# Kernel optimization log

Measured on AMD Instinct MI355X. Metric: run time of the kernel, lower is better.

The kernel has to match this reference:

```python
import jax, jax.numpy as jnp
import numpy as np

B = 512        # number of graphs in the batch
NP = 512       # nodes per graph (max segment length)
N = B * NP     # total nodes
D = 256        # in_feats
K = 32         # top-k nodes kept per graph


def setup_inputs() -> dict:
    key = jax.random.key(0)
    k1, k2 = jax.random.split(key, 2)
    feat = jax.random.normal(k1, (N, D), dtype=jnp.float32)
    w = jax.random.normal(k2, (1, D), dtype=jnp.float32) / np.sqrt(D)  # nn.Linear(in_feats, 1) weight
    b = jnp.zeros((1,), dtype=jnp.float32)                              # nn.Linear bias
    segment_ids = jnp.repeat(jnp.arange(B, dtype=jnp.int32), NP)        # sorted graph id per node
    return {"feat": feat, "w": w, "b": b, "segment_ids": segment_ids}


def reference(feat, w, b, segment_ids):
    # gate = self.att(feat) -> (N, 1) -> (N,)
    gate = (feat @ w.T + b)[:, 0]

    # dgl.softmax_nodes: numerically stable segment softmax per graph
    gmax = jax.ops.segment_max(gate, segment_ids, num_segments=B)
    e = jnp.exp(gate - gmax[segment_ids])
    denom = jax.ops.segment_sum(e, segment_ids, num_segments=B)
    gate_sm = e / denom[segment_ids]                                    # (N,)

    # position of each node within its segment (supports ragged segments)
    counts = jax.ops.segment_sum(jnp.ones((N,), jnp.int32), segment_ids, num_segments=B)
    offsets = jnp.concatenate([jnp.zeros((1,), jnp.int32), jnp.cumsum(counts)[:-1].astype(jnp.int32)])
    pos = jnp.arange(N, dtype=jnp.int32) - offsets[segment_ids]

    # scatter gates into dense (B, NP) padded with -inf, keep node ids alongside
    neg_inf = jnp.finfo(jnp.float32).min
    dense_gate = jnp.full((B, NP), neg_inf, jnp.float32).at[segment_ids, pos].set(gate_sm)
    dense_nid = jnp.zeros((B, NP), jnp.int32).at[segment_ids, pos].set(jnp.arange(N, dtype=jnp.int32))

    # dgl.topk_nodes: per-graph top-k by gate, gather node features -> (B, K, D)
    _, cols = jax.lax.top_k(dense_gate, K)
    node_idx = jnp.take_along_axis(dense_nid, cols, axis=1)             # (B, K) global node ids
    return feat[node_idx]                                               # (B, K, D)
```

## Files before the change

### kernel.cpp

```cpp
#include <hip/hip_runtime.h>

#define D   256
#define NP  512
#define BG  512
#define K   32
#define D4  (D/4)

__global__ __launch_bounds__(256) void gate_kernel(const float* __restrict__ feat,
                                                   const float* __restrict__ w,
                                                   const float* __restrict__ b,
                                                   float* __restrict__ gate,
                                                   int n_rows) {
    const int lane   = threadIdx.x & 63;
    const int wave   = (blockIdx.x * blockDim.x + threadIdx.x) >> 6;
    const int nwaves = (gridDim.x * blockDim.x) >> 6;

    const float4 w4  = ((const float4*)w)[lane];
    const float bias = b[0];
    const float4* f4 = (const float4*)feat;

    for (int row = wave; row < n_rows; row += nwaves) {
        float4 f = f4[(size_t)row * D4 + lane];
        float s = f.x * w4.x + f.y * w4.y + f.z * w4.z + f.w * w4.w;
        #pragma unroll
        for (int off = 32; off; off >>= 1)
            s += __shfl_xor(s, off, 64);
        if (lane == 0) gate[row] = s + bias;
    }
}

__global__ __launch_bounds__(256) void topk_kernel(const float* __restrict__ feat,
                                                   const float* __restrict__ gate,
                                                   float* __restrict__ out) {
    __shared__ float sval[NP];
    __shared__ int   sidx[NP];
    __shared__ float red[4];
    __shared__ float s_bcast;

    const int g    = blockIdx.x;
    const int tid  = threadIdx.x;
    const int lane = tid & 63;
    const int wid  = tid >> 6;

    const float v0 = gate[g * NP + tid];
    const float v1 = gate[g * NP + tid + 256];

    float m = fmaxf(v0, v1);
    #pragma unroll
    for (int off = 32; off; off >>= 1)
        m = fmaxf(m, __shfl_xor(m, off, 64));
    if (lane == 0) red[wid] = m;
    __syncthreads();
    if (tid == 0) s_bcast = fmaxf(fmaxf(red[0], red[1]), fmaxf(red[2], red[3]));
    __syncthreads();
    const float gmax = s_bcast;

    const float e0 = expf(v0 - gmax);
    const float e1 = expf(v1 - gmax);
    float s = e0 + e1;
    #pragma unroll
    for (int off = 32; off; off >>= 1)
        s += __shfl_xor(s, off, 64);
    __syncthreads();
    if (lane == 0) red[wid] = s;
    __syncthreads();
    if (tid == 0) s_bcast = (red[0] + red[1]) + (red[2] + red[3]);
    __syncthreads();
    const float denom = s_bcast;

    sval[tid]        = e0 / denom;  sidx[tid]        = tid;
    sval[tid + 256]  = e1 / denom;  sidx[tid + 256]  = tid + 256;
    __syncthreads();

    for (int k = 2; k <= NP; k <<= 1) {
        for (int j = k >> 1; j > 0; j >>= 1) {
            #pragma unroll
            for (int rep = 0; rep < 2; ++rep) {
                int t = tid + rep * 256;
                int ixj = t ^ j;
                if (ixj > t) {
                    float va = sval[t],  vb = sval[ixj];
                    int   ia = sidx[t],  ib = sidx[ixj];
                    bool b_first = (vb > va) || (vb == va && ib < ia);
                    bool do_swap = ((t & k) == 0) ? b_first : !b_first;
                    if (do_swap) {
                        sval[t] = vb; sval[ixj] = va;
                        sidx[t] = ib; sidx[ixj] = ia;
                    }
                }
            }
            __syncthreads();
        }
    }

    const float4* f4 = (const float4*)feat;
    float4*       o4 = (float4*)out;
    #pragma unroll
    for (int q = tid; q < K * D4; q += 256) {
        int r = q >> 6;
        int c = q & 63;
        int node = g * NP + sidx[r];
        o4[((size_t)(g * K + r)) * D4 + c] = f4[(size_t)node * D4 + c];
    }
}

extern "C" void kernel_launch(void* const* d_in, const int* in_sizes, int n_in,
                              void* d_out, int out_size, void* d_ws, size_t ws_size,
                              hipStream_t stream) {
    const float* feat = (const float*)d_in[0];
    const float* w    = (const float*)d_in[1];
    const float* b    = (const float*)d_in[2];

    const int n_rows = in_sizes[0] / D;
    float* gate = (float*)d_ws;
    float* out  = (float*)d_out;

    gate_kernel<<<2048, 256, 0, stream>>>(feat, w, b, gate, n_rows);
    topk_kernel<<<BG, 256, 0, stream>>>(feat, gate, out);
}
```

Before: 378.3 us.

## Fuse gate GEMV and top-k into one kernel using wave-level bitonic merges

Replaces the separate gate kernel and shared-memory bitonic sort with one kernel per graph. Each of 8 waves computes 64 gate scores in registers, sorts them with shuffle-based bitonic networks, and a tree of top-32 merges combines the waves. The softmax and bias are dropped because both are monotonic and do not change which nodes rank highest. This removes the gate round-trip through global memory, the second launch and the many barriers of the 512-element sort. Ties in the gate values could order differently, and only one block per graph reads all of that graph's features.

```diff
diff --git a/kernel.cpp b/kernel.cpp
--- a/kernel.cpp
+++ b/kernel.cpp
@@ -1,106 +1,111 @@
 #include <hip/hip_runtime.h>
 
-#define D   256
-#define NP  512
-#define BG  512
-#define K   32
-#define D4  (D/4)
+#define D    256
+#define NP   512
+#define BG   512
+#define K    32
+#define D4   (D/4)
 
-__global__ __launch_bounds__(256) void gate_kernel(const float* __restrict__ feat,
-                                                   const float* __restrict__ w,
-                                                   const float* __restrict__ b,
-                                                   float* __restrict__ gate,
-                                                   int n_rows) {
-    const int lane   = threadIdx.x & 63;
-    const int wave   = (blockIdx.x * blockDim.x + threadIdx.x) >> 6;
-    const int nwaves = (gridDim.x * blockDim.x) >> 6;
-
-    const float4 w4  = ((const float4*)w)[lane];
-    const float bias = b[0];
-    const float4* f4 = (const float4*)feat;
-
-    for (int row = wave; row < n_rows; row += nwaves) {
-        float4 f = f4[(size_t)row * D4 + lane];
-        float s = f.x * w4.x + f.y * w4.y + f.z * w4.z + f.w * w4.w;
-        #pragma unroll
-        for (int off = 32; off; off >>= 1)
-            s += __shfl_xor(s, off, 64);
-        if (lane == 0) gate[row] = s + bias;
+__device__ __forceinline__ void bitonic_merge64(int lane, float& v, int& idx) {
+    #pragma unroll
+    for (int j = 32; j > 0; j >>= 1) {
+        float ov = __shfl_xor(v, j, 64);
+        int   oi = __shfl_xor(idx, j, 64);
+        bool mg = (v > ov) || (v == ov && idx < oi);
+        if (mg != ((lane & j) == 0)) { v = ov; idx = oi; }
     }
 }
 
-__global__ __launch_bounds__(256) void topk_kernel(const float* __restrict__ feat,
-                                                   const float* __restrict__ gate,
-                                                   float* __restrict__ out) {
-    __shared__ float sval[NP];
-    __shared__ int   sidx[NP];
-    __shared__ float red[4];
-    __shared__ float s_bcast;
+__global__ __launch_bounds__(512) void fused_topk(const float* __restrict__ feat,
+                                                  const float* __restrict__ w,
+                                                  float* __restrict__ out) {
+    __shared__ float mv[14 * K];
+    __shared__ int   mi[14 * K];
+    __shared__ int   sfin[K];
 
     const int g    = blockIdx.x;
     const int tid  = threadIdx.x;
     const int lane = tid & 63;
     const int wid  = tid >> 6;
 
-    const float v0 = gate[g * NP + tid];
-    const float v1 = gate[g * NP + tid + 256];
+    const float4  w4 = ((const float4*)w)[lane];
+    const float4* f4 = (const float4*)feat + (size_t)g * NP * D4;
 
-    float m = fmaxf(v0, v1);
+    const int rbase = wid * 64;
+    float myv = 0.0f;
+    #pragma unroll 4
+    for (int i0 = 0; i0 < 64; i0 += 4) {
+        float4 f0 = f4[(size_t)(rbase + i0 + 0) * D4 + lane];
+        float4 f1 = f4[(size_t)(rbase + i0 + 1) * D4 + lane];
+        float4 f2 = f4[(size_t)(rbase + i0 + 2) * D4 + lane];
+        float4 f3 = f4[(size_t)(rbase + i0 + 3) * D4 + lane];
+        float s0 = f0.x*w4.x + f0.y*w4.y + f0.z*w4.z + f0.w*w4.w;
+        float s1 = f1.x*w4.x + f1.y*w4.y + f1.z*w4.z + f1.w*w4.w;
+        float s2 = f2.x*w4.x + f2.y*w4.y + f2.z*w4.z + f2.w*w4.w;
+        float s3 = f3.x*w4.x + f3.y*w4.y + f3.z*w4.z + f3.w*w4.w;
+        #pragma unroll
+        for (int off = 32; off; off >>= 1) {
+            s0 += __shfl_xor(s0, off, 64);
+            s1 += __shfl_xor(s1, off, 64);
+            s2 += __shfl_xor(s2, off, 64);
+            s3 += __shfl_xor(s3, off, 64);
+        }
+        if (lane == i0 + 0) myv = s0;
+        if (lane == i0 + 1) myv = s1;
+        if (lane == i0 + 2) myv = s2;
+        if (lane == i0 + 3) myv = s3;
+    }
+
+    float v  = myv;
+    int  idx = rbase + lane;
     #pragma unroll
-    for (int off = 32; off; off >>= 1)
-        m = fmaxf(m, __shfl_xor(m, off, 64));
-    if (lane == 0) red[wid] = m;
-    __syncthreads();
-    if (tid == 0) s_bcast = fmaxf(fmaxf(red[0], red[1]), fmaxf(red[2], red[3]));
-    __syncthreads();
-    const float gmax = s_bcast;
+    for (int k = 2; k < 64; k <<= 1) {
+        #pragma unroll
+        for (int j = k >> 1; j > 0; j >>= 1) {
+            float ov = __shfl_xor(v, j, 64);
+            int   oi = __shfl_xor(idx, j, 64);
+            bool mg  = (v > ov) || (v == ov && idx < oi);
+            bool dir = ((lane & k) == 0);
+            if (mg != (((lane & j) == 0) == dir)) { v = ov; idx = oi; }
+        }
+    }
+    bitonic_merge64(lane, v, idx);
 
-    const float e0 = expf(v0 - gmax);
-    const float e1 = expf(v1 - gmax);
-    float s = e0 + e1;
-    #pragma unroll
-    for (int off = 32; off; off >>= 1)
-        s += __shfl_xor(s, off, 64);
-    __syncthreads();
-    if (lane == 0) red[wid] = s;
-    __syncthreads();
-    if (tid == 0) s_bcast = (red[0] + red[1]) + (red[2] + red[3]);
-    __syncthreads();
-    const float denom = s_bcast;
-
-    sval[tid]        = e0 / denom;  sidx[tid]        = tid;
-    sval[tid + 256]  = e1 / denom;  sidx[tid + 256]  = tid + 256;
+    if (lane < K) { mv[wid * K + lane] = v; mi[wid * K + lane] = idx; }
     __syncthreads();
 
-    for (int k = 2; k <= NP; k <<= 1) {
-        for (int j = k >> 1; j > 0; j >>= 1) {
-            #pragma unroll
-            for (int rep = 0; rep < 2; ++rep) {
-                int t = tid + rep * 256;
-                int ixj = t ^ j;
-                if (ixj > t) {
-                    float va = sval[t],  vb = sval[ixj];
-                    int   ia = sidx[t],  ib = sidx[ixj];
-                    bool b_first = (vb > va) || (vb == va && ib < ia);
-                    bool do_swap = ((t & k) == 0) ? b_first : !b_first;
-                    if (do_swap) {
-                        sval[t] = vb; sval[ixj] = va;
-                        sidx[t] = ib; sidx[ixj] = ia;
-                    }
-                }
-            }
-            __syncthreads();
-        }
+    if (wid < 4) {
+        int a = 2 * wid, b = 2 * wid + 1;
+        int pos = (lane < K) ? (a * K + lane) : (b * K + (63 - lane));
+        float v1 = mv[pos]; int i1 = mi[pos];
+        bitonic_merge64(lane, v1, i1);
+        if (lane < K) { mv[(8 + wid) * K + lane] = v1; mi[(8 + wid) * K + lane] = i1; }
     }
+    __syncthreads();
+    if (wid < 2) {
+        int a = 8 + 2 * wid, b = 9 + 2 * wid;
+        int pos = (lane < K) ? (a * K + lane) : (b * K + (63 - lane));
+        float v1 = mv[pos]; int i1 = mi[pos];
+        bitonic_merge64(lane, v1, i1);
+        if (lane < K) { mv[(12 + wid) * K + lane] = v1; mi[(12 + wid) * K + lane] = i1; }
+    }
+    __syncthreads();
+    if (wid == 0) {
+        int pos = (lane < K) ? (12 * K + lane) : (13 * K + (63 - lane));
+        float v1 = mv[pos]; int i1 = mi[pos];
+        bitonic_merge64(lane, v1, i1);
+        if (lane < K) sfin[lane] = i1;
+    }
+    __syncthreads();
 
-    const float4* f4 = (const float4*)feat;
-    float4*       o4 = (float4*)out;
+    float4* o4 = (float4*)out + (size_t)g * K * D4;
     #pragma unroll
-    for (int q = tid; q < K * D4; q += 256) {
+    for (int it = 0; it < (K * D4) / 512; ++it) {
+        int q = tid + it * 512;
         int r = q >> 6;
         int c = q & 63;
-        int node = g * NP + sidx[r];
-        o4[((size_t)(g * K + r)) * D4 + c] = f4[(size_t)node * D4 + c];
+        int node = sfin[r];
+        o4[(size_t)r * D4 + c] = f4[(size_t)node * D4 + c];
     }
 }
 
@@ -109,12 +114,7 @@
                               hipStream_t stream) {
     const float* feat = (const float*)d_in[0];
     const float* w    = (const float*)d_in[1];
-    const float* b    = (const float*)d_in[2];
+    float* out = (float*)d_out;
 
-    const int n_rows = in_sizes[0] / D;
-    float* gate = (float*)d_ws;
-    float* out  = (float*)d_out;
-
-    gate_kernel<<<2048, 256, 0, stream>>>(feat, w, b, gate, n_rows);
-    topk_kernel<<<BG, 256, 0, stream>>>(feat, gate, out);
+    fused_topk<<<BG, 512, 0, stream>>>(feat, w, out);
 }
```

Result: no change. 372.0 us (-1.7%).
